# Kernel tuning notes

Hardware: AMD Instinct MI355X
Metric: run time of the kernel (lower is better)

## Reference

```python
import jax, jax.numpy as jnp
import numpy as np
import math

HGT, WID = 24, 24          # shape2d
NUM_HEADS = 12
EMB = 768
HEAD_DIM = EMB // NUM_HEADS
N_GRID = HGT * WID         # 576 spatial tokens
N_TOK = N_GRID + 1         # +1 CLS token
BATCH = 32


def _rel_indices(h: int, w: int) -> np.ndarray:
    """[(h*w), (h*w)] indices into the (2h-1)*(2w-1) relative table."""
    y = np.arange(h)
    x = np.arange(w)
    y1, x1, y2, x2 = np.meshgrid(y, x, y, x, indexing='ij')
    idx = (y1 - y2 + h - 1) * (2 * w - 1) + (x1 - x2 + w - 1)
    return idx.reshape(h * w, h * w)


def setup_inputs() -> dict:
    key = jax.random.key(0)
    ks = jax.random.split(key, 6)
    s = 0.02
    return {
        "x": jax.random.normal(ks[0], (BATCH, N_TOK, EMB), dtype=jnp.float32),
        "Wq": jax.random.normal(ks[1], (EMB, EMB), dtype=jnp.float32) * s,
        "bq": jnp.zeros((EMB,), dtype=jnp.float32),
        "Wk": jax.random.normal(ks[2], (EMB, EMB), dtype=jnp.float32) * s,
        "bk": jnp.zeros((EMB,), dtype=jnp.float32),
        "Wv": jax.random.normal(ks[3], (EMB, EMB), dtype=jnp.float32) * s,
        "bv": jnp.zeros((EMB,), dtype=jnp.float32),
        "Wp": jax.random.normal(ks[4], (EMB, EMB), dtype=jnp.float32) * s,
        "bp": jnp.zeros((EMB,), dtype=jnp.float32),
        "rel_table": jax.random.normal(ks[5], ((2 * HGT - 1) * (2 * WID - 1), NUM_HEADS), dtype=jnp.float32) * s,
    }


def reference(x, Wq, bq, Wk, bk, Wv, bv, Wp, bp, rel_table):
    B, N, E = x.shape
    scale = 1.0 / math.sqrt(HEAD_DIM)

    def heads(t):  # [B,N,E] -> [B,H,N,hd]
        return t.reshape(B, N, NUM_HEADS, HEAD_DIM).transpose(0, 2, 1, 3)

    q = heads(x @ Wq.T + bq)
    k = heads(x @ Wk.T + bk)
    v = heads(x @ Wv.T + bv)

    scores = jnp.einsum('bhqd,bhkd->bhqk', q, k) * scale  # [B,H,N,N]

    # relative position bias on spatial tokens (skip CLS row/col)
    idx = jnp.asarray(_rel_indices(HGT, WID))              # [Ng,Ng]
    bias = rel_table[idx].transpose(2, 0, 1)               # [H,Ng,Ng]
    scores = scores.at[:, :, 1:, 1:].add(bias)

    attn = jax.nn.softmax(scores, axis=-1)
    out = jnp.einsum('bhqk,bhkd->bhqd', attn, v)           # [B,H,N,hd]
    out = out.transpose(0, 2, 1, 3).reshape(B, N, E)
    return out @ Wp.T + bp
```

## Files before the change

### kernel.cpp

```cpp
#include <hip/hip_runtime.h>
#include <hip/hip_bf16.h>
#include <stdint.h>

#define HGT   24
#define WID   24
#define NHEAD 12
#define EMB   768
#define HD    64
#define NGRID 576
#define NTOK  577
#define NPAD  640
#define BATCH 32
#define MROWS (BATCH * NTOK)
#define NKT   10
#define NIT   5
#define NQT   5
#define QKVC  (3 * EMB)

typedef __attribute__((ext_vector_type(8))) short bf16x8;
typedef __attribute__((ext_vector_type(4))) float f32x4;

__device__ __forceinline__ short f2bf(float f) {
    union { float f; unsigned u; } c; c.f = f;
    unsigned r = (c.u + 0x7FFFu + ((c.u >> 16) & 1u)) >> 16;
    return (short)(r & 0xFFFFu);
}
__device__ __forceinline__ float b2f(short s) {
    union { unsigned u; float f; } c; c.u = ((unsigned)(unsigned short)s) << 16;
    return c.f;
}
__device__ __forceinline__ unsigned pk2bf(float a, float b) {
    __hip_bfloat162 h = __float22bfloat162_rn(make_float2(a, b));
    union { __hip_bfloat162 h; unsigned u; } c; c.h = h;
    return c.u;
}
__device__ __forceinline__ float fexp2(float x) {
#if __has_builtin(__builtin_amdgcn_exp2f)
    return __builtin_amdgcn_exp2f(x);
#else
    return __expf(x * 0.69314718f);
#endif
}

__device__ __forceinline__ void gload16(void* lds, const void* g) {
    __builtin_amdgcn_global_load_lds(
        (const __attribute__((address_space(1))) void*)g,
        (__attribute__((address_space(3))) void*)lds, 16, 0, 0);
}

__device__ __forceinline__ void wait_vm0_barrier() {
    asm volatile("s_waitcnt vmcnt(0)" ::: "memory");
    __builtin_amdgcn_s_barrier();
}

__device__ __forceinline__ int xcd_swizzle(int orig, int nwg) {
    int q = nwg >> 3, r = nwg & 7;
    int xcd = orig & 7, idx = orig >> 3;
    return (xcd < r) ? xcd * (q + 1) + idx : r * (q + 1) + (xcd - r) * q + idx;
}

__global__ void cast_f32_bf16(const float* __restrict__ src, short* __restrict__ dst, int n) {
    int i = (blockIdx.x * blockDim.x + threadIdx.x) * 4;
    int stride = gridDim.x * blockDim.x * 4;
    for (int j = i; j < n; j += stride) {
        float4 v = *(const float4*)(src + j);
        uint2 o;
        o.x = pk2bf(v.x, v.y);
        o.y = pk2bf(v.z, v.w);
        *(uint2*)(dst + j) = o;
    }
}

__global__ void bias_expand(const float* __restrict__ rel, short* __restrict__ be) {
    const float L2E = 1.44269504f;
    int q = blockIdx.x;
    int k = threadIdx.x;
    float v[NHEAD];
    if (k >= NTOK) {
#pragma unroll
        for (int h = 0; h < NHEAD; h++) v[h] = -1e30f;
    } else if (q == 0 || q >= NTOK || k == 0) {
#pragma unroll
        for (int h = 0; h < NHEAD; h++) v[h] = 0.f;
    } else {
        int i = q - 1, j = k - 1;
        int idx = ((i / WID) - (j / WID) + HGT - 1) * (2 * WID - 1)
                + ((i % WID) - (j % WID) + WID - 1);
        const float* rp = rel + (size_t)idx * NHEAD;
#pragma unroll
        for (int h = 0; h < NHEAD; h++) v[h] = rp[h];
    }
#pragma unroll
    for (int h = 0; h < NHEAD; h++)
        be[((size_t)h * NPAD + q) * NPAD + k] = f2bf(v[h] * L2E);
}

template <int MODE>
__global__ __launch_bounds__(512) void gemm_bt(
    const short* __restrict__ A, const short* __restrict__ Bw,
    const float* __restrict__ b0, const float* __restrict__ b1, const float* __restrict__ b2,
    void* __restrict__ Outp, short* __restrict__ vout, int M)
{
    constexpr int NC  = (MODE == 0) ? QKVC : EMB;
    constexpr int NBX = NC / 256;
    constexpr int K   = EMB;
    constexpr int NST = K / 32;

    __shared__ __align__(16) short Asl[4][256][32];
    __shared__ __align__(16) short Bsl[4][256][32];

    const int t    = threadIdx.x;
    const int lane = t & 63;
    const int w    = t >> 6;
    const int wm   = w >> 2;
    const int wn   = w & 3;
    const int lg   = lane >> 4;
    const int li   = lane & 15;

    const int nwg  = NBX * ((MROWS + 255) / 256);
    const int wgid = xcd_swizzle(blockIdx.x, nwg);
    const int tm   = (wgid / NBX) * 256;
    const int tn   = (wgid % NBX) * 256;

    const int drow = lane >> 2;
    const int lc   = (lane & 3) ^ ((lane >> 3) & 3);
    const int xsw  = (li >> 1) & 3;

    const short* agp[2];
    const short* bgp[2];
#pragma unroll
    for (int gi = 0; gi < 2; gi++) {
        int rm = tm + gi * 128 + w * 16 + drow; if (rm >= M) rm = M - 1;
        agp[gi] = A  + (size_t)rm * K + lc * 8;
        bgp[gi] = Bw + (size_t)(tn + gi * 128 + w * 16 + drow) * K + lc * 8;
    }

    f32x4 acc[8][4];
#pragma unroll
    for (int i = 0; i < 8; i++)
#pragma unroll
        for (int j = 0; j < 4; j++) acc[i][j] = (f32x4){0.f, 0.f, 0.f, 0.f};

#pragma unroll
    for (int ss = 0; ss < 3; ss++) {
        gload16(&Asl[ss][0 * 128 + w * 16][0], agp[0] + ss * 32);
        gload16(&Asl[ss][1 * 128 + w * 16][0], agp[1] + ss * 32);
        gload16(&Bsl[ss][0 * 128 + w * 16][0], bgp[0] + ss * 32);
        gload16(&Bsl[ss][1 * 128 + w * 16][0], bgp[1] + ss * 32);
    }

    for (int s = 0; s < NST; s++) {
        if (s < NST - 2)       asm volatile("s_waitcnt vmcnt(8)" ::: "memory");
        else if (s == NST - 2) asm volatile("s_waitcnt vmcnt(4)" ::: "memory");
        else                   asm volatile("s_waitcnt vmcnt(0)" ::: "memory");
        __builtin_amdgcn_s_barrier();

        const int cb = s & 3;
        bf16x8 af[8], bfv[4];
#pragma unroll
        for (int mi = 0; mi < 8; mi++)
            af[mi] = *(const bf16x8*)&Asl[cb][wm * 128 + mi * 16 + li][(lg ^ xsw) * 8];
#pragma unroll
        for (int nj = 0; nj < 4; nj++)
            bfv[nj] = *(const bf16x8*)&Bsl[cb][wn * 64 + nj * 16 + li][(lg ^ xsw) * 8];

        if (s + 3 < NST) {
            const int tb = (s + 3) & 3;
            const int ko = (s + 3) * 32;
            gload16(&Asl[tb][0 * 128 + w * 16][0], agp[0] + ko);
            gload16(&Asl[tb][1 * 128 + w * 16][0], agp[1] + ko);
            gload16(&Bsl[tb][0 * 128 + w * 16][0], bgp[0] + ko);
            gload16(&Bsl[tb][1 * 128 + w * 16][0], bgp[1] + ko);
        }

        __builtin_amdgcn_s_setprio(1);
#pragma unroll
        for (int mi = 0; mi < 8; mi++)
#pragma unroll
            for (int nj = 0; nj < 4; nj++)
                acc[mi][nj] = __builtin_amdgcn_mfma_f32_16x16x32_bf16(
                    bfv[nj], af[mi], acc[mi][nj], 0, 0, 0);
        __builtin_amdgcn_s_setprio(0);
    }

    if (MODE == 0 && tn >= 2 * EMB) {
#pragma unroll
        for (int nj = 0; nj < 4; nj++) {
            const int ccb = tn + wn * 64 + nj * 16 + lg * 4;
            const int e   = ccb - 2 * EMB;
            const int hh  = e >> 6, db = e & 63;
            const float4 bias4 = *(const float4*)&b2[e];
#pragma unroll
            for (int mi = 0; mi < 8; mi++) {
                int m = tm + wm * 128 + mi * 16 + li;
                if (m >= M) continue;
                int bi = m / NTOK;
                int n  = m - bi * NTOK;
                short* vr = vout + (((size_t)bi * NHEAD + hh) * HD + db) * NPAD + n;
                vr[0 * NPAD] = f2bf(acc[mi][nj][0] + bias4.x);
                vr[1 * NPAD] = f2bf(acc[mi][nj][1] + bias4.y);
                vr[2 * NPAD] = f2bf(acc[mi][nj][2] + bias4.z);
                vr[3 * NPAD] = f2bf(acc[mi][nj][3] + bias4.w);
            }
        }
    } else {
#pragma unroll
        for (int nj = 0; nj < 4; nj++) {
            const int ccb = tn + wn * 64 + nj * 16 + lg * 4;
            float4 bias4;
            if constexpr (MODE == 0) {
                int which = (ccb >= EMB) ? 1 : 0;
                const float* bb = (which == 0) ? b0 : b1;
                bias4 = *(const float4*)&bb[ccb - which * EMB];
            } else {
                bias4 = *(const float4*)&b0[ccb];
            }
#pragma unroll
            for (int mi = 0; mi < 8; mi++) {
                int m = tm + wm * 128 + mi * 16 + li;
                if (m >= M) continue;
                if constexpr (MODE == 0) {
                    uint2 o;
                    o.x = pk2bf(acc[mi][nj][0] + bias4.x, acc[mi][nj][1] + bias4.y);
                    o.y = pk2bf(acc[mi][nj][2] + bias4.z, acc[mi][nj][3] + bias4.w);
                    *(uint2*)&((short*)Outp)[(size_t)m * NC + ccb] = o;
                } else {
                    float4 o;
                    o.x = acc[mi][nj][0] + bias4.x;
                    o.y = acc[mi][nj][1] + bias4.y;
                    o.z = acc[mi][nj][2] + bias4.z;
                    o.w = acc[mi][nj][3] + bias4.w;
                    *(float4*)&((float*)Outp)[(size_t)m * NC + ccb] = o;
                }
            }
        }
    }
}

__global__ __launch_bounds__(256) void attn_kernel(
    const short* __restrict__ qnat, const short* __restrict__ vt,
    const short* __restrict__ biasx, short* __restrict__ aout)
{
    __shared__ __align__(16) short Ksl[2][2][64][64];
    __shared__ __align__(16) short Vsl[2][2][64][64];
    __shared__ __align__(16) short Psl[4][16][64];

    const int wg = (blockIdx.x & 7) * (BATCH * NHEAD * NQT / 8) + (blockIdx.x >> 3);
    const int qt = wg % NQT;
    const int rest = wg / NQT;
    const int b  = rest & 31;
    const int h  = rest >> 5;

    const int t    = threadIdx.x;
    const int lane = t & 63;
    const int w    = t >> 6;
    const int lg   = lane >> 4;
    const int li   = lane & 15;
    const int xh   = li & 7;
    const int qbase = qt * 128;
    const int myq[2] = { qbase + w * 32 + li, qbase + w * 32 + 16 + li };

    const float SCL = 0.18033688f;

    const short* qp  = qnat + (size_t)b * NTOK * QKVC + h * HD;
    const short* kp  = qp + EMB;
    const short* vtp = vt + ((size_t)b * NHEAD + h) * (size_t)HD * NPAD;
    const short* browq[2] = { biasx + ((size_t)h * NPAD + myq[0]) * NPAD,
                              biasx + ((size_t)h * NPAD + myq[1]) * NPAD };

    bf16x8 qf[2][2];
#pragma unroll
    for (int q2 = 0; q2 < 2; q2++) {
        int qrow = myq[q2] < NTOK ? myq[q2] : NTOK - 1;
        qf[q2][0] = *(const bf16x8*)(qp + (size_t)qrow * QKVC + lg * 8);
        qf[q2][1] = *(const bf16x8*)(qp + (size_t)qrow * QKVC + 32 + lg * 8);
    }

    float mrun[2] = { -1e30f, -1e30f }, lrun[2] = { 0.f, 0.f };
    f32x4 oacc[2][4];
#pragma unroll
    for (int q2 = 0; q2 < 2; q2++)
#pragma unroll
        for (int d = 0; d < 4; d++) oacc[q2][d] = (f32x4){0.f, 0.f, 0.f, 0.f};

    const int srow = w * 8 + (lane >> 3);
    const int cofs = ((lane & 7) ^ (lane >> 3)) * 8;

#pragma unroll
    for (int st = 0; st < 2; st++)
#pragma unroll
        for (int p = 0; p < 2; p++) {
            int key = st * 64 + p * 32 + srow; if (key >= NTOK) key = NTOK - 1;
            gload16(&Ksl[0][st][p * 32 + w * 8][0], kp + (size_t)key * QKVC + cofs);
            gload16(&Vsl[0][st][p * 32 + w * 8][0],
                    vtp + (size_t)(p * 32 + srow) * NPAD + st * 64 + cofs);
        }
    short4 bcur[2][2][4];
#pragma unroll
    for (int q2 = 0; q2 < 2; q2++)
#pragma unroll
        for (int st = 0; st < 2; st++)
#pragma unroll
            for (int j = 0; j < 4; j++)
                bcur[q2][st][j] = *(const short4*)&browq[q2][st * 64 + j * 16 + lg * 4];
    wait_vm0_barrier();

    for (int it = 0; it < NIT; it++) {
        const int cb = it & 1, nb = cb ^ 1;

        if (it + 1 < NIT) {
#pragma unroll
            for (int st = 0; st < 2; st++)
#pragma unroll
                for (int p = 0; p < 2; p++) {
                    int key = (it + 1) * 128 + st * 64 + p * 32 + srow;
                    if (key >= NTOK) key = NTOK - 1;
                    gload16(&Ksl[nb][st][p * 32 + w * 8][0], kp + (size_t)key * QKVC + cofs);
                    gload16(&Vsl[nb][st][p * 32 + w * 8][0],
                            vtp + (size_t)(p * 32 + srow) * NPAD + (it + 1) * 128 + st * 64 + cofs);
                }
        }

        float pvv[2][2][4][4];
        __builtin_amdgcn_s_setprio(1);
#pragma unroll
        for (int st = 0; st < 2; st++) {
#pragma unroll
            for (int j = 0; j < 4; j++) {
                bf16x8 ak0 = *(const bf16x8*)&Ksl[cb][st][j * 16 + li][(lg ^ xh) * 8];
                bf16x8 ak1 = *(const bf16x8*)&Ksl[cb][st][j * 16 + li][((4 + lg) ^ xh) * 8];
#pragma unroll
                for (int q2 = 0; q2 < 2; q2++) {
                    f32x4 s = (f32x4){0.f, 0.f, 0.f, 0.f};
                    s = __builtin_amdgcn_mfma_f32_16x16x32_bf16(ak0, qf[q2][0], s, 0, 0, 0);
                    s = __builtin_amdgcn_mfma_f32_16x16x32_bf16(ak1, qf[q2][1], s, 0, 0, 0);
                    pvv[st][q2][j][0] = fmaf(s[0], SCL, b2f(bcur[q2][st][j].x));
                    pvv[st][q2][j][1] = fmaf(s[1], SCL, b2f(bcur[q2][st][j].y));
                    pvv[st][q2][j][2] = fmaf(s[2], SCL, b2f(bcur[q2][st][j].z));
                    pvv[st][q2][j][3] = fmaf(s[3], SCL, b2f(bcur[q2][st][j].w));
                }
            }
        }
        __builtin_amdgcn_s_setprio(0);

        float mt[2];
#pragma unroll
        for (int q2 = 0; q2 < 2; q2++) {
            float m = pvv[0][q2][0][0];
#pragma unroll
            for (int st = 0; st < 2; st++)
#pragma unroll
                for (int j = 0; j < 4; j++)
#pragma unroll
                    for (int r = 0; r < 4; r++) m = fmaxf(m, pvv[st][q2][j][r]);
            m = fmaxf(m, __shfl_xor(m, 16, 64));
            m = fmaxf(m, __shfl_xor(m, 32, 64));
            mt[q2] = m;
        }
        bool need = (mt[0] > mrun[0] + 8.0f) || (mt[1] > mrun[1] + 8.0f);
        if (__any(need)) {
#pragma unroll
            for (int q2 = 0; q2 < 2; q2++) {
                float nm  = fmaxf(mrun[q2], mt[q2]);
                float fac = fexp2(mrun[q2] - nm);
                mrun[q2] = nm;
                lrun[q2] *= fac;
#pragma unroll
                for (int d = 0; d < 4; d++) oacc[q2][d] *= fac;
            }
        }
#pragma unroll
        for (int q2 = 0; q2 < 2; q2++) {
            float rs = 0.f;
#pragma unroll
            for (int st = 0; st < 2; st++)
#pragma unroll
                for (int j = 0; j < 4; j++)
#pragma unroll
                    for (int r = 0; r < 4; r++) {
                        float p = fexp2(pvv[st][q2][j][r] - mrun[q2]);
                        pvv[st][q2][j][r] = p;
                        rs += p;
                    }
            rs += __shfl_xor(rs, 16, 64);
            rs += __shfl_xor(rs, 32, 64);
            lrun[q2] += rs;
        }

#pragma unroll
        for (int st = 0; st < 2; st++) {
            bf16x8 av[4][2];
#pragma unroll
            for (int dd = 0; dd < 4; dd++)
#pragma unroll
                for (int kk = 0; kk < 2; kk++)
                    av[dd][kk] = *(const bf16x8*)&Vsl[cb][st][dd * 16 + li][((kk * 4 + lg) ^ xh) * 8];
#pragma unroll
            for (int q2 = 0; q2 < 2; q2++) {
#pragma unroll
                for (int j = 0; j < 4; j++) {
                    uint2 pw;
                    pw.x = pk2bf(pvv[st][q2][j][0], pvv[st][q2][j][1]);
                    pw.y = pk2bf(pvv[st][q2][j][2], pvv[st][q2][j][3]);
                    *(uint2*)&Psl[w][li][(((2 * j + (lg >> 1)) ^ xh) * 8) + (lg & 1) * 4] = pw;
                }
                bf16x8 pb[2];
#pragma unroll
                for (int kk = 0; kk < 2; kk++)
                    pb[kk] = *(const bf16x8*)&Psl[w][li][((kk * 4 + lg) ^ xh) * 8];
                __builtin_amdgcn_s_setprio(1);
#pragma unroll
                for (int dd = 0; dd < 4; dd++)
#pragma unroll
                    for (int kk = 0; kk < 2; kk++)
                        oacc[q2][dd] = __builtin_amdgcn_mfma_f32_16x16x32_bf16(
                            av[dd][kk], pb[kk], oacc[q2][dd], 0, 0, 0);
                __builtin_amdgcn_s_setprio(0);
            }
        }

        short4 bnxt[2][2][4];
        {
            int itn = (it + 1 < NIT) ? it + 1 : it;
#pragma unroll
            for (int q2 = 0; q2 < 2; q2++)
#pragma unroll
                for (int st = 0; st < 2; st++)
#pragma unroll
                    for (int j = 0; j < 4; j++)
                        bnxt[q2][st][j] =
                            *(const short4*)&browq[q2][(itn * 2 + st) * 64 + j * 16 + lg * 4];
        }

        wait_vm0_barrier();
#pragma unroll
        for (int q2 = 0; q2 < 2; q2++)
#pragma unroll
            for (int st = 0; st < 2; st++)
#pragma unroll
                for (int j = 0; j < 4; j++) bcur[q2][st][j] = bnxt[q2][st][j];
    }

#pragma unroll
    for (int q2 = 0; q2 < 2; q2++) {
        if (myq[q2] < NTOK) {
            float inv = 1.0f / lrun[q2];
            short* op = aout + ((size_t)b * NTOK + myq[q2]) * EMB + h * HD;
#pragma unroll
            for (int dd = 0; dd < 4; dd++) {
                uint2 o;
                o.x = pk2bf(oacc[q2][dd][0] * inv, oacc[q2][dd][1] * inv);
                o.y = pk2bf(oacc[q2][dd][2] * inv, oacc[q2][dd][3] * inv);
                *(uint2*)&op[dd * 16 + lg * 4] = o;
            }
        }
    }
}

extern "C" void kernel_launch(void* const* d_in, const int* in_sizes, int n_in,
                              void* d_out, int out_size, void* d_ws, size_t ws_size,
                              hipStream_t stream) {
    (void)in_sizes; (void)n_in; (void)out_size; (void)ws_size;
    const float* x   = (const float*)d_in[0];
    const float* Wq  = (const float*)d_in[1];
    const float* bq  = (const float*)d_in[2];
    const float* Wk  = (const float*)d_in[3];
    const float* bk  = (const float*)d_in[4];
    const float* Wv  = (const float*)d_in[5];
    const float* bv  = (const float*)d_in[6];
    const float* Wp  = (const float*)d_in[7];
    const float* bp  = (const float*)d_in[8];
    const float* rel = (const float*)d_in[9];

    const size_t WN = (size_t)EMB * EMB;
    short* Wb   = (short*)d_ws;
    short* Wpb  = Wb + 3 * WN;
    short* qnat = Wpb + WN;
    short* xb   = qnat + (size_t)MROWS * QKVC;
    short* aout = xb;
    short* vtb  = xb + (size_t)MROWS * EMB;
    short* bexp = vtb + (size_t)BATCH * NHEAD * HD * NPAD;

    const int XN = MROWS * EMB;
    const int MT = (MROWS + 255) / 256;
    cast_f32_bf16<<<576, 256, 0, stream>>>(Wq, Wb, (int)WN);
    cast_f32_bf16<<<576, 256, 0, stream>>>(Wk, Wb + WN, (int)WN);
    cast_f32_bf16<<<576, 256, 0, stream>>>(Wv, Wb + 2 * WN, (int)WN);
    cast_f32_bf16<<<576, 256, 0, stream>>>(Wp, Wpb, (int)WN);
    cast_f32_bf16<<<13848, 256, 0, stream>>>(x, xb, XN);
    bias_expand<<<NPAD, NPAD, 0, stream>>>(rel, bexp);

    gemm_bt<0><<<9 * MT, 512, 0, stream>>>(xb, Wb, bq, bk, bv, qnat, vtb, MROWS);
    attn_kernel<<<BATCH * NHEAD * NQT, 256, 0, stream>>>(qnat, vtb, bexp, aout);
    gemm_bt<1><<<3 * MT, 512, 0, stream>>>(aout, Wpb, bp, bp, bp, d_out, nullptr, MROWS);
}
```

Measured before the change: 299.6 us.

## Widen attention blocks to 256 queries with 8 waves and fuse cast kernels

The attention kernel now runs 512 threads per block and covers 256 query rows, so each K/V tile staged in LDS serves twice as many queries. This cuts redundant K/V global loads and the block count (3 query tiles instead of 5). Each wave now loads one 8-row slice instead of two. The third tile is mostly padding, and bias rows are clamped to stay in bounds. Separately, the five f32-to-bf16 cast launches are merged into one kernel to reduce launch overhead.

After: 324.7 us. +8.4%, slower.

```diff
diff --git a/kernel.cpp b/kernel.cpp
--- a/kernel.cpp
+++ b/kernel.cpp
@@ -12,9 +12,8 @@
 #define NPAD  640
 #define BATCH 32
 #define MROWS (BATCH * NTOK)
-#define NKT   10
 #define NIT   5
-#define NQT   5
+#define NQT3  3
 #define QKVC  (3 * EMB)
 
 typedef __attribute__((ext_vector_type(8))) short bf16x8;
@@ -59,16 +58,31 @@
     return (xcd < r) ? xcd * (q + 1) + idx : r * (q + 1) + (xcd - r) * q + idx;
 }
 
-__global__ void cast_f32_bf16(const float* __restrict__ src, short* __restrict__ dst, int n) {
-    int i = (blockIdx.x * blockDim.x + threadIdx.x) * 4;
-    int stride = gridDim.x * blockDim.x * 4;
-    for (int j = i; j < n; j += stride) {
-        float4 v = *(const float4*)(src + j);
-        uint2 o;
-        o.x = pk2bf(v.x, v.y);
-        o.y = pk2bf(v.z, v.w);
-        *(uint2*)(dst + j) = o;
-    }
+__global__ void cast_all(const float* __restrict__ x,
+                         const float* __restrict__ Wq, const float* __restrict__ Wk,
+                         const float* __restrict__ Wv, const float* __restrict__ Wp,
+                         short* __restrict__ xb, short* __restrict__ Wb, short* __restrict__ Wpb) {
+    const size_t WN = (size_t)EMB * EMB;
+    int bid = blockIdx.x;
+    const float* src;
+    short* dst;
+    int local;
+    if (bid < 13848) {
+        src = x; dst = xb; local = bid;
+    } else {
+        int s = (bid - 13848) / 576;
+        local = (bid - 13848) - s * 576;
+        if (s == 0)      { src = Wq; dst = Wb; }
+        else if (s == 1) { src = Wk; dst = Wb + WN; }
+        else if (s == 2) { src = Wv; dst = Wb + 2 * WN; }
+        else             { src = Wp; dst = Wpb; }
+    }
+    int j = (local * 256 + threadIdx.x) * 4;
+    float4 v = *(const float4*)(src + j);
+    uint2 o;
+    o.x = pk2bf(v.x, v.y);
+    o.y = pk2bf(v.z, v.w);
+    *(uint2*)(dst + j) = o;
 }
 
 __global__ void bias_expand(const float* __restrict__ rel, short* __restrict__ be) {
@@ -237,17 +251,17 @@
     }
 }
 
-__global__ __launch_bounds__(256) void attn_kernel(
+__global__ __launch_bounds__(512) void attn_kernel(
     const short* __restrict__ qnat, const short* __restrict__ vt,
     const short* __restrict__ biasx, short* __restrict__ aout)
 {
     __shared__ __align__(16) short Ksl[2][2][64][64];
     __shared__ __align__(16) short Vsl[2][2][64][64];
-    __shared__ __align__(16) short Psl[4][16][64];
-
-    const int wg = (blockIdx.x & 7) * (BATCH * NHEAD * NQT / 8) + (blockIdx.x >> 3);
-    const int qt = wg % NQT;
-    const int rest = wg / NQT;
+    __shared__ __align__(16) short Psl[8][16][64];
+
+    const int wg = (blockIdx.x & 7) * (BATCH * NHEAD * NQT3 / 8) + (blockIdx.x >> 3);
+    const int qt = wg % NQT3;
+    const int rest = wg / NQT3;
     const int b  = rest & 31;
     const int h  = rest >> 5;
 
@@ -257,7 +271,7 @@
     const int lg   = lane >> 4;
     const int li   = lane & 15;
     const int xh   = li & 7;
-    const int qbase = qt * 128;
+    const int qbase = qt * 256;
     const int myq[2] = { qbase + w * 32 + li, qbase + w * 32 + 16 + li };
 
     const float SCL = 0.18033688f;
@@ -265,8 +279,9 @@
     const short* qp  = qnat + (size_t)b * NTOK * QKVC + h * HD;
     const short* kp  = qp + EMB;
     const short* vtp = vt + ((size_t)b * NHEAD + h) * (size_t)HD * NPAD;
-    const short* browq[2] = { biasx + ((size_t)h * NPAD + myq[0]) * NPAD,
-                              biasx + ((size_t)h * NPAD + myq[1]) * NPAD };
+    const short* browq[2] = {
+        biasx + ((size_t)h * NPAD + (myq[0] < NPAD ? myq[0] : NPAD - 1)) * NPAD,
+        biasx + ((size_t)h * NPAD + (myq[1] < NPAD ? myq[1] : NPAD - 1)) * NPAD };
 
     bf16x8 qf[2][2];
 #pragma unroll
@@ -287,14 +302,11 @@
     const int cofs = ((lane & 7) ^ (lane >> 3)) * 8;
 
 #pragma unroll
-    for (int st = 0; st < 2; st++)
-#pragma unroll
-        for (int p = 0; p < 2; p++) {
-            int key = st * 64 + p * 32 + srow; if (key >= NTOK) key = NTOK - 1;
-            gload16(&Ksl[0][st][p * 32 + w * 8][0], kp + (size_t)key * QKVC + cofs);
-            gload16(&Vsl[0][st][p * 32 + w * 8][0],
-                    vtp + (size_t)(p * 32 + srow) * NPAD + st * 64 + cofs);
-        }
+    for (int st = 0; st < 2; st++) {
+        int key = st * 64 + srow; if (key >= NTOK) key = NTOK - 1;
+        gload16(&Ksl[0][st][w * 8][0], kp + (size_t)key * QKVC + cofs);
+        gload16(&Vsl[0][st][w * 8][0], vtp + (size_t)srow * NPAD + st * 64 + cofs);
+    }
     short4 bcur[2][2][4];
 #pragma unroll
     for (int q2 = 0; q2 < 2; q2++)
@@ -310,15 +322,12 @@
 
         if (it + 1 < NIT) {
 #pragma unroll
-            for (int st = 0; st < 2; st++)
-#pragma unroll
-                for (int p = 0; p < 2; p++) {
-                    int key = (it + 1) * 128 + st * 64 + p * 32 + srow;
-                    if (key >= NTOK) key = NTOK - 1;
-                    gload16(&Ksl[nb][st][p * 32 + w * 8][0], kp + (size_t)key * QKVC + cofs);
-                    gload16(&Vsl[nb][st][p * 32 + w * 8][0],
-                            vtp + (size_t)(p * 32 + srow) * NPAD + (it + 1) * 128 + st * 64 + cofs);
-                }
+            for (int st = 0; st < 2; st++) {
+                int key = (it + 1) * 128 + st * 64 + srow; if (key >= NTOK) key = NTOK - 1;
+                gload16(&Ksl[nb][st][w * 8][0], kp + (size_t)key * QKVC + cofs);
+                gload16(&Vsl[nb][st][w * 8][0],
+                        vtp + (size_t)srow * NPAD + (it + 1) * 128 + st * 64 + cofs);
+            }
         }
 
         float pvv[2][2][4][4];
@@ -481,16 +490,11 @@
     short* vtb  = xb + (size_t)MROWS * EMB;
     short* bexp = vtb + (size_t)BATCH * NHEAD * HD * NPAD;
 
-    const int XN = MROWS * EMB;
     const int MT = (MROWS + 255) / 256;
-    cast_f32_bf16<<<576, 256, 0, stream>>>(Wq, Wb, (int)WN);
-    cast_f32_bf16<<<576, 256, 0, stream>>>(Wk, Wb + WN, (int)WN);
-    cast_f32_bf16<<<576, 256, 0, stream>>>(Wv, Wb + 2 * WN, (int)WN);
-    cast_f32_bf16<<<576, 256, 0, stream>>>(Wp, Wpb, (int)WN);
-    cast_f32_bf16<<<13848, 256, 0, stream>>>(x, xb, XN);
+    cast_all<<<13848 + 4 * 576, 256, 0, stream>>>(x, Wq, Wk, Wv, Wp, xb, Wb, Wpb);
     bias_expand<<<NPAD, NPAD, 0, stream>>>(rel, bexp);
 
     gemm_bt<0><<<9 * MT, 512, 0, stream>>>(xb, Wb, bq, bk, bv, qnat, vtb, MROWS);
-    attn_kernel<<<BATCH * NHEAD * NQT, 256, 0, stream>>>(qnat, vtb, bexp, aout);
+    attn_kernel<<<BATCH * NHEAD * NQT3, 512, 0, stream>>>(qnat, vtb, bexp, aout);
     gemm_bt<1><<<3 * MT, 512, 0, stream>>>(aout, Wpb, bp, bp, bp, d_out, nullptr, MROWS);
 }
```
